# Optimization experiments

Hardware: AMD Instinct MI355X
Metric: run time of the kernel (lower is better)

Reference implementation:

```python
import jax, jax.numpy as jnp
import numpy as np

S = 4  # spixel_downsize


def _shift2d(x, oy, ox):
    # out[..., y, x] = x[..., y - oy, x - ox] if in-bounds else 0 (zero pad)
    pad = [(0, 0)] * (x.ndim - 2) + [(S, S), (S, S)]
    xp = jnp.pad(x, pad)
    h, w = x.shape[-2], x.shape[-1]
    return xp[..., S - oy:S - oy + h, S - ox:S - ox + w]


def _valid_mask(h, w, oy, ox):
    ys = jnp.arange(h)
    xs = jnp.arange(w)
    my = (ys - oy >= 0) & (ys - oy < h)
    mx = (xs - ox >= 0) & (xs - ox < w)
    return my[:, None] & mx[None, :]


def _conv3d(x, w, stride, pad):
    return jax.lax.conv_general_dilated(
        x, w, window_strides=stride, padding=[(p, p) for p in pad],
        dimension_numbers=('NCDHW', 'OIDHW', 'NCDHW'))


def _basic(x, w, stride, pad):
    # BasicConv: Conv3d(bias=False) + BN(identity at init) + ReLU
    return jax.nn.relu(_conv3d(x, w, stride, pad))


def setup_inputs() -> dict:
    key = jax.random.key(0)
    ks = jax.random.split(key, 8)
    cv = jax.random.normal(ks[0], (1, 8, 24, 128, 256), jnp.float32)
    sp = jax.random.uniform(ks[1], (1, 9, 128, 256), jnp.float32)
    xy = jax.random.normal(ks[2], (1, 2, 128, 256), jnp.float32)
    w_stem = jax.random.normal(ks[3], (16, 72, 1, 1, 1), jnp.float32) * 0.05
    w1a = jax.random.normal(ks[4], (32, 16, 3, 2, 2), jnp.float32) * 0.05
    w1b = jax.random.normal(ks[5], (32, 32, 3, 1, 1), jnp.float32) * 0.05
    w2a = jax.random.normal(ks[6], (64, 32, 3, 2, 2), jnp.float32) * 0.05
    w2b = jax.random.normal(ks[7], (64, 64, 3, 1, 1), jnp.float32) * 0.05
    return dict(cv=cv, sp=sp, xy=xy, w_stem=w_stem, w1a=w1a, w1b=w1b, w2a=w2a, w2b=w2b)


def reference(cv, sp, xy, w_stem, w1a, w1b, w2a, w2b):
    b, c, d, h, w = cv.shape
    feats, probs = [], []
    uv0 = jnp.zeros((b, 2, h, w), cv.dtype)
    # 9 shifted neighbors; neighbor k shifts by (S*((k//3)-1), S*((k%3)-1)).
    # All uv writes in the original target slot 0 and sequentially overwrite;
    for k in range(9):
        oy = S * ((k // 3) - 1)
        ox = S * ((k % 3) - 1)
        p = _shift2d(sp[:, k], oy, ox)                      # (b,h,w), zeros outside
        probs.append(p)
        feats.append(_shift2d(cv, oy, ox) * p[:, None, None])  # (b,c,d,h,w)
        u = _shift2d(xy, oy, ox) * p[:, None]               # (b,2,h,w)
        mask = _valid_mask(h, w, oy, ox)[None, None]
        uv0 = jnp.where(mask, u, uv0)
    # (b, c, 9, d, h, w) -> (b, 9c, d, h, w), matching torch reshape order
    feat = jnp.stack(feats, axis=2).reshape(b, c * 9, d, h, w)
    prob_sum = jnp.sum(jnp.stack(probs, axis=1), axis=1, keepdims=True)  # (b,1,h,w)
    tot = prob_sum.reshape(b, 1, h // S, S, w // S, S).mean((3, 5))      # avg_pool2d
    tot_up = jnp.repeat(jnp.repeat(tot, S, axis=2), S, axis=3)           # nearest upsample
    feat = feat / tot_up[:, :, None]                                     # (b,9c,d,h,w)
    feat = _basic(feat, w_stem, (1, 1, 1), (0, 0, 0))
    f1 = _basic(feat, w1a, (2, 2, 2), (1, 0, 0))
    f1 = _basic(f1, w1b, (1, 1, 1), (1, 0, 0))
    f2 = _basic(f1, w2a, (2, 2, 2), (1, 0, 0))
    f2 = _basic(f2, w2b, (1, 1, 1), (1, 0, 0))
    # uv.sum(2) == uv0 since only neighbor-slot 0 is written
    uv = uv0.reshape(b, 2, h // S, S, w // S, S).mean((3, 5)) / tot      # (b,2,h/S,w/S)
    return f1, f2, uv.reshape(b, 2, -1)
```

## Files before the change

### kernel.cpp

```cpp
#include <hip/hip_runtime.h>

#define HH 128
#define WW 256

#define OFF_TOT   0
#define OFF_WT    2048
#define WT_STEM   0
#define WT_1A     1152
#define WT_1B     7296
#define WT_2A     10368
#define WT_2B     34944
#define OFF_STEM  49280
#define OFF_F1A   12632192
#define OFF_F1N   15777920
#define OFF_F2A   49280

__global__ __launch_bounds__(256) void k_pre(
    const float* __restrict__ sp, const float* __restrict__ xy,
    const float* __restrict__ wstem, const float* __restrict__ w1a,
    const float* __restrict__ w1b, const float* __restrict__ w2a,
    const float* __restrict__ w2b,
    float* __restrict__ tot, float* __restrict__ uv_out, float* __restrict__ wt)
{
  int gid = blockIdx.x * 256 + threadIdx.x;
  if (gid < 1152) { int o = gid & 15, r = gid >> 4; int ci = r / 9, k = r - ci * 9;
    wt[WT_STEM + gid] = wstem[o * 72 + ci * 9 + k]; }
  if (gid < 6144) { int o = gid & 31, ci = (gid >> 5) & 15, tp = gid >> 9;
    wt[WT_1A + gid] = w1a[o * 192 + ci * 12 + tp]; }
  if (gid < 3072) { int o = gid & 31, ci = (gid >> 5) & 31, kd = gid >> 10;
    wt[WT_1B + gid] = w1b[(o * 32 + ci) * 3 + kd]; }
  if (gid < 24576) { int o = gid & 63, ci = (gid >> 6) & 31, tp = gid >> 11;
    wt[WT_2A + gid] = w2a[o * 384 + ci * 12 + tp]; }
  if (gid < 12288) { int o = gid & 63, ci = (gid >> 6) & 63, kd = gid >> 12;
    wt[WT_2B + gid] = w2b[(o * 64 + ci) * 3 + kd]; }
  if (gid < 8192) {
    int cell = gid >> 2, q = gid & 3;
    int Y = cell >> 6, X = cell & 63;
    float tsum = 0.f, u0 = 0.f, u1 = 0.f;
    int y = Y * 4 + q;
#pragma unroll
    for (int j = 0; j < 4; ++j) {
      int x = X * 4 + j;
      float psum = 0.f;
#pragma unroll
      for (int k = 0; k < 9; ++k) {
        int oy = 4 * ((k / 3) - 1), ox = 4 * ((k % 3) - 1);
        int sy = y - oy, sx = x - ox;
        if (sy >= 0 && sy < HH && sx >= 0 && sx < WW)
          psum += sp[k * HH * WW + sy * WW + sx];
      }
      tsum += psum;
      int oy = (y >= 4) ? 4 : 0;
      int ox = (x >= 4) ? 4 : 0;
      int kk = (oy ? 2 : 1) * 3 + (ox ? 2 : 1);
      int sy = y - oy, sx = x - ox;
      float p = sp[kk * HH * WW + sy * WW + sx];
      u0 += xy[sy * WW + sx] * p;
      u1 += xy[HH * WW + sy * WW + sx] * p;
    }
    tsum += __shfl_xor(tsum, 1); tsum += __shfl_xor(tsum, 2);
    u0 += __shfl_xor(u0, 1); u0 += __shfl_xor(u0, 2);
    u1 += __shfl_xor(u1, 1); u1 += __shfl_xor(u1, 2);
    if (q == 0) {
      float t = tsum * (1.f / 16.f);
      tot[cell] = t;
      float inv = 1.f / t;
      uv_out[cell] = u0 * (1.f / 16.f) * inv;
      uv_out[2048 + cell] = u1 * (1.f / 16.f) * inv;
    }
  }
}

__global__ __launch_bounds__(256) void k_stem(
    const float* __restrict__ cv, const float* __restrict__ sp,
    const float* __restrict__ wt, const float* __restrict__ tot,
    float* __restrict__ out)
{
  __shared__ float wl[1152];
  for (int i = threadIdx.x; i < 1152; i += 256) wl[i] = wt[i];
  __syncthreads();
  int x0 = blockIdx.x * 128 + 2 * (threadIdx.x & 63);
  int y  = blockIdx.y * 4 + (threadIdx.x >> 6);
  int d  = blockIdx.z;
  float2 p2[9]; int off[9];
#pragma unroll
  for (int k = 0; k < 9; ++k) {
    int oy = 4 * ((k / 3) - 1), ox = 4 * ((k % 3) - 1);
    int sy = y - oy, sx = x0 - ox;
    bool v = (sy >= 0) && (sy < HH) && (sx >= 0) && (sx < WW - 1);
    int syc = v ? sy : 0, sxc = v ? sx : 0;
    off[k] = syc * WW + sxc;
    float2 t = *(const float2*)(sp + k * HH * WW + off[k]);
    p2[k].x = v ? t.x : 0.f;
    p2[k].y = v ? t.y : 0.f;
  }
  float acc[16][2];
#pragma unroll
  for (int o = 0; o < 16; ++o) { acc[o][0] = 0.f; acc[o][1] = 0.f; }
  const float* cvd = cv + (size_t)d * HH * WW;
#pragma unroll
  for (int ci = 0; ci < 8; ++ci) {
    const float* cvp = cvd + (size_t)ci * 24 * HH * WW;
    float2 c2[9];
#pragma unroll
    for (int k = 0; k < 9; ++k) c2[k] = *(const float2*)(cvp + off[k]);
#pragma unroll
    for (int k = 0; k < 9; ++k) {
      float t0 = c2[k].x * p2[k].x, t1 = c2[k].y * p2[k].y;
      const float* wb = &wl[(ci * 9 + k) * 16];
      float wv[16];
#pragma unroll
      for (int q = 0; q < 4; ++q) *(float4*)&wv[q * 4] = *(const float4*)(wb + q * 4);
#pragma unroll
      for (int o = 0; o < 16; ++o) {
        acc[o][0] += wv[o] * t0;
        acc[o][1] += wv[o] * t1;
      }
    }
  }
  float inv = 1.f / tot[(y >> 2) * 64 + (x0 >> 2)];
  float* op = out + (((size_t)d * HH + y) * WW + x0) * 16;
#pragma unroll
  for (int p = 0; p < 2; ++p)
#pragma unroll
    for (int q = 0; q < 4; ++q) {
      float4 v;
      v.x = fmaxf(acc[q * 4 + 0][p] * inv, 0.f);
      v.y = fmaxf(acc[q * 4 + 1][p] * inv, 0.f);
      v.z = fmaxf(acc[q * 4 + 2][p] * inv, 0.f);
      v.w = fmaxf(acc[q * 4 + 3][p] * inv, 0.f);
      *(float4*)(op + p * 16 + q * 4) = v;
    }
}

__global__ __launch_bounds__(256) void k_conv1a(
    const float* __restrict__ in, const float* __restrict__ wt,
    float* __restrict__ out)
{
  __shared__ float wl[6144];
  for (int i = threadIdx.x; i < 6144; i += 256) wl[i] = wt[i];
  __syncthreads();
  int tid = threadIdx.x;
  int xo0 = (blockIdx.x & 1) * 64 + 2 * (tid & 31);
  int yo  = (blockIdx.x >> 1) * 8 + (tid >> 5);
  int dz = blockIdx.y, og = blockIdx.z;
  float acc[16][2];
#pragma unroll
  for (int o = 0; o < 16; ++o) { acc[o][0] = 0.f; acc[o][1] = 0.f; }
  for (int kd = 0; kd < 3; ++kd) {
    int d = 2 * dz - 1 + kd;
    if (d < 0 || d >= 24) continue;
#pragma unroll
    for (int ky = 0; ky < 2; ++ky) {
      int y = 2 * yo + ky;
      float iv[64];
      const float4* ip = (const float4*)(in + (((size_t)d * 128 + y) * 256 + 2 * xo0) * 16);
#pragma unroll
      for (int q = 0; q < 16; ++q) {
        float4 v = ip[q];
        iv[q * 4 + 0] = v.x; iv[q * 4 + 1] = v.y;
        iv[q * 4 + 2] = v.z; iv[q * 4 + 3] = v.w;
      }
#pragma unroll
      for (int kx = 0; kx < 2; ++kx) {
        const float* wtap = &wl[((kd * 2 + ky) * 2 + kx) * 512 + og * 16];
#pragma unroll
        for (int ci = 0; ci < 16; ++ci) {
          const float* wb = wtap + ci * 32;
          float wv[16];
#pragma unroll
          for (int q = 0; q < 4; ++q) *(float4*)&wv[q * 4] = *(const float4*)(wb + q * 4);
          float a0 = iv[(0 + kx) * 16 + ci];
          float a1 = iv[(2 + kx) * 16 + ci];
#pragma unroll
          for (int o = 0; o < 16; ++o) {
            acc[o][0] += wv[o] * a0;
            acc[o][1] += wv[o] * a1;
          }
        }
      }
    }
  }
  float* op = out + (((size_t)dz * 64 + yo) * 128 + xo0) * 32 + og * 16;
#pragma unroll
  for (int p = 0; p < 2; ++p)
#pragma unroll
    for (int q = 0; q < 4; ++q) {
      float4 v;
      v.x = fmaxf(acc[q * 4 + 0][p], 0.f);
      v.y = fmaxf(acc[q * 4 + 1][p], 0.f);
      v.z = fmaxf(acc[q * 4 + 2][p], 0.f);
      v.w = fmaxf(acc[q * 4 + 3][p], 0.f);
      *(float4*)(op + p * 32 + q * 4) = v;
    }
}

__global__ __launch_bounds__(256) void k_conv1b(
    const float* __restrict__ in, const float* __restrict__ wt,
    float* __restrict__ outn, float* __restrict__ outc)
{
  __shared__ float wl[3072];
  for (int i = threadIdx.x; i < 3072; i += 256) wl[i] = wt[i];
  __syncthreads();
  int tid = threadIdx.x;
  int xo = (blockIdx.x & 1) * 64 + (tid & 63);
  int yo = (blockIdx.x >> 1) * 4 + (tid >> 6);
  int dz = blockIdx.y, og = blockIdx.z;
  float acc[16];
#pragma unroll
  for (int o = 0; o < 16; ++o) acc[o] = 0.f;
  for (int kd = 0; kd < 3; ++kd) {
    int d = dz - 1 + kd;
    if (d < 0 || d >= 12) continue;
    float iv[32];
    const float4* ip = (const float4*)(in + (((size_t)d * 64 + yo) * 128 + xo) * 32);
#pragma unroll
    for (int q = 0; q < 8; ++q) {
      float4 v = ip[q];
      iv[q * 4 + 0] = v.x; iv[q * 4 + 1] = v.y;
      iv[q * 4 + 2] = v.z; iv[q * 4 + 3] = v.w;
    }
    const float* wk = &wl[kd * 1024 + og * 16];
#pragma unroll
    for (int ci = 0; ci < 32; ++ci) {
      const float* wb = wk + ci * 32;
      float wv[16];
#pragma unroll
      for (int q = 0; q < 4; ++q) *(float4*)&wv[q * 4] = *(const float4*)(wb + q * 4);
#pragma unroll
      for (int o = 0; o < 16; ++o) acc[o] += wv[o] * iv[ci];
    }
  }
  float* onp = outn + (((size_t)dz * 64 + yo) * 128 + xo) * 32 + og * 16;
#pragma unroll
  for (int q = 0; q < 4; ++q) {
    float4 v;
    v.x = fmaxf(acc[q * 4 + 0], 0.f);
    v.y = fmaxf(acc[q * 4 + 1], 0.f);
    v.z = fmaxf(acc[q * 4 + 2], 0.f);
    v.w = fmaxf(acc[q * 4 + 3], 0.f);
    *(float4*)(onp + q * 4) = v;
  }
#pragma unroll
  for (int o = 0; o < 16; ++o)
    outc[((size_t)((og * 16 + o) * 12 + dz) * 64 + yo) * 128 + xo] = fmaxf(acc[o], 0.f);
}

__global__ __launch_bounds__(256) void k_conv2a(
    const float* __restrict__ in, const float* __restrict__ wt,
    float* __restrict__ out)
{
  __shared__ float wl[3072];
  int og = blockIdx.z;
  for (int i = threadIdx.x; i < 3072; i += 256) {
    int o = i & 7, ci = (i >> 3) & 31, tap = i >> 8;
    wl[i] = wt[tap * 2048 + ci * 64 + og * 8 + o];
  }
  __syncthreads();
  int tid = threadIdx.x;
  int xo = tid & 63;
  int yo = blockIdx.x * 4 + (tid >> 6);
  int dz = blockIdx.y;
  float acc[8];
#pragma unroll
  for (int o = 0; o < 8; ++o) acc[o] = 0.f;
  for (int kd = 0; kd < 3; ++kd) {
    int d = 2 * dz - 1 + kd;
    if (d < 0 || d >= 12) continue;
#pragma unroll
    for (int ky = 0; ky < 2; ++ky) {
      int y = 2 * yo + ky;
      float iv[64];
      const float4* ip = (const float4*)(in + (((size_t)d * 64 + y) * 128 + 2 * xo) * 32);
#pragma unroll
      for (int q = 0; q < 16; ++q) {
        float4 v = ip[q];
        iv[q * 4 + 0] = v.x; iv[q * 4 + 1] = v.y;
        iv[q * 4 + 2] = v.z; iv[q * 4 + 3] = v.w;
      }
#pragma unroll
      for (int kx = 0; kx < 2; ++kx) {
        const float* wtap = &wl[((kd * 2 + ky) * 2 + kx) * 256];
#pragma unroll
        for (int ci = 0; ci < 32; ++ci) {
          const float* wb = wtap + ci * 8;
          float wv[8];
          *(float4*)&wv[0] = *(const float4*)(wb);
          *(float4*)&wv[4] = *(const float4*)(wb + 4);
          float a = iv[kx * 32 + ci];
#pragma unroll
          for (int o = 0; o < 8; ++o) acc[o] += wv[o] * a;
        }
      }
    }
  }
  float* op = out + (((size_t)dz * 32 + yo) * 64 + xo) * 64 + og * 8;
  float4 v0, v1;
  v0.x = fmaxf(acc[0], 0.f); v0.y = fmaxf(acc[1], 0.f);
  v0.z = fmaxf(acc[2], 0.f); v0.w = fmaxf(acc[3], 0.f);
  v1.x = fmaxf(acc[4], 0.f); v1.y = fmaxf(acc[5], 0.f);
  v1.z = fmaxf(acc[6], 0.f); v1.w = fmaxf(acc[7], 0.f);
  *(float4*)op = v0; *(float4*)(op + 4) = v1;
}

__global__ __launch_bounds__(256) void k_conv2b(
    const float* __restrict__ in, const float* __restrict__ wt,
    float* __restrict__ out)
{
  __shared__ float wl[1536];
  int og = blockIdx.z;
  for (int i = threadIdx.x; i < 1536; i += 256) {
    int o = i & 7, ci = (i >> 3) & 63, kd = i >> 9;
    wl[i] = wt[kd * 4096 + ci * 64 + og * 8 + o];
  }
  __syncthreads();
  int tid = threadIdx.x;
  int xo = tid & 63;
  int yo = blockIdx.x * 4 + (tid >> 6);
  int dz = blockIdx.y;
  float acc[8];
#pragma unroll
  for (int o = 0; o < 8; ++o) acc[o] = 0.f;
  for (int kd = 0; kd < 3; ++kd) {
    int d = dz - 1 + kd;
    if (d < 0 || d >= 6) continue;
    float iv[64];
    const float4* ip = (const float4*)(in + (((size_t)d * 32 + yo) * 64 + xo) * 64);
#pragma unroll
    for (int q = 0; q < 16; ++q) {
      float4 v = ip[q];
      iv[q * 4 + 0] = v.x; iv[q * 4 + 1] = v.y;
      iv[q * 4 + 2] = v.z; iv[q * 4 + 3] = v.w;
    }
    const float* wk = &wl[kd * 512];
#pragma unroll
    for (int ci = 0; ci < 64; ++ci) {
      const float* wb = wk + ci * 8;
      float wv[8];
      *(float4*)&wv[0] = *(const float4*)(wb);
      *(float4*)&wv[4] = *(const float4*)(wb + 4);
#pragma unroll
      for (int o = 0; o < 8; ++o) acc[o] += wv[o] * iv[ci];
    }
  }
#pragma unroll
  for (int o = 0; o < 8; ++o)
    out[((size_t)((og * 8 + o) * 6 + dz) * 32 + yo) * 64 + xo] = fmaxf(acc[o], 0.f);
}

extern "C" void kernel_launch(void* const* d_in, const int* in_sizes, int n_in,
                              void* d_out, int out_size, void* d_ws, size_t ws_size,
                              hipStream_t stream) {
  const float* cv    = (const float*)d_in[0];
  const float* sp    = (const float*)d_in[1];
  const float* xy    = (const float*)d_in[2];
  const float* wstem = (const float*)d_in[3];
  const float* w1a   = (const float*)d_in[4];
  const float* w1b   = (const float*)d_in[5];
  const float* w2a   = (const float*)d_in[6];
  const float* w2b   = (const float*)d_in[7];
  float* out = (float*)d_out;
  float* out_f1 = out;
  float* out_f2 = out + 3145728;
  float* out_uv = out + 3145728 + 786432;

  float* ws = (float*)d_ws;
  float* t_tot  = ws + OFF_TOT;
  float* wt     = ws + OFF_WT;
  float* t_stem = ws + OFF_STEM;
  float* t_f1a  = ws + OFF_F1A;
  float* t_f1n  = ws + OFF_F1N;
  float* t_f2a  = ws + OFF_F2A;

  k_pre<<<96, 256, 0, stream>>>(sp, xy, wstem, w1a, w1b, w2a, w2b,
                                t_tot, out_uv, wt);
  k_stem<<<dim3(2, 32, 24), 256, 0, stream>>>(cv, sp, wt + WT_STEM, t_tot, t_stem);
  k_conv1a<<<dim3(16, 12, 2), 256, 0, stream>>>(t_stem, wt + WT_1A, t_f1a);
  k_conv1b<<<dim3(32, 12, 2), 256, 0, stream>>>(t_f1a, wt + WT_1B, t_f1n, out_f1);
  k_conv2a<<<dim3(8, 6, 8), 256, 0, stream>>>(t_f1n, wt + WT_2A, t_f2a);
  k_conv2b<<<dim3(8, 6, 8), 256, 0, stream>>>(t_f2a, wt + WT_2B, out_f2);
}
```

Before: 174.7 us.

## Double-buffer input loads and split output channels across more blocks in conv kernels

Every conv kernel now prefetches the next input slice into registers (a double-buffered `ib[2][32]`) while the current slice is multiplied. The stem kernel does the same across its input channels. Output channels per thread are halved in all four convs (1a: 16→8, 1b: 16→8, 2a/2b: 8→4), and the grids grow to match. This gives more parallelism and lower register pressure, which should raise occupancy and hide load latency, at the cost of rereading each input once per extra channel group.

```diff
diff --git a/kernel.cpp b/kernel.cpp
--- a/kernel.cpp
+++ b/kernel.cpp
@@ -2,6 +2,7 @@
 
 #define HH 128
 #define WW 256
+#define HW (HH * WW)
 
 #define OFF_TOT   0
 #define OFF_WT    2048
@@ -47,16 +48,16 @@
         int oy = 4 * ((k / 3) - 1), ox = 4 * ((k % 3) - 1);
         int sy = y - oy, sx = x - ox;
         if (sy >= 0 && sy < HH && sx >= 0 && sx < WW)
-          psum += sp[k * HH * WW + sy * WW + sx];
+          psum += sp[k * HW + sy * WW + sx];
       }
       tsum += psum;
       int oy = (y >= 4) ? 4 : 0;
       int ox = (x >= 4) ? 4 : 0;
       int kk = (oy ? 2 : 1) * 3 + (ox ? 2 : 1);
       int sy = y - oy, sx = x - ox;
-      float p = sp[kk * HH * WW + sy * WW + sx];
+      float p = sp[kk * HW + sy * WW + sx];
       u0 += xy[sy * WW + sx] * p;
-      u1 += xy[HH * WW + sy * WW + sx] * p;
+      u1 += xy[HW + sy * WW + sx] * p;
     }
     tsum += __shfl_xor(tsum, 1); tsum += __shfl_xor(tsum, 2);
     u0 += __shfl_xor(u0, 1); u0 += __shfl_xor(u0, 2);
@@ -90,23 +91,28 @@
     bool v = (sy >= 0) && (sy < HH) && (sx >= 0) && (sx < WW - 1);
     int syc = v ? sy : 0, sxc = v ? sx : 0;
     off[k] = syc * WW + sxc;
-    float2 t = *(const float2*)(sp + k * HH * WW + off[k]);
+    float2 t = *(const float2*)(sp + k * HW + off[k]);
     p2[k].x = v ? t.x : 0.f;
     p2[k].y = v ? t.y : 0.f;
   }
   float acc[16][2];
 #pragma unroll
   for (int o = 0; o < 16; ++o) { acc[o][0] = 0.f; acc[o][1] = 0.f; }
-  const float* cvd = cv + (size_t)d * HH * WW;
+  const float* cvd = cv + (size_t)d * HW;
+  float2 cb[2][9];
+#pragma unroll
+  for (int k = 0; k < 9; ++k) cb[0][k] = *(const float2*)(cvd + off[k]);
 #pragma unroll
   for (int ci = 0; ci < 8; ++ci) {
-    const float* cvp = cvd + (size_t)ci * 24 * HH * WW;
-    float2 c2[9];
-#pragma unroll
-    for (int k = 0; k < 9; ++k) c2[k] = *(const float2*)(cvp + off[k]);
+    if (ci < 7) {
+#pragma unroll
+      for (int k = 0; k < 9; ++k)
+        cb[(ci + 1) & 1][k] = *(const float2*)(cvd + (size_t)(ci + 1) * 24 * HW + off[k]);
+    }
 #pragma unroll
     for (int k = 0; k < 9; ++k) {
-      float t0 = c2[k].x * p2[k].x, t1 = c2[k].y * p2[k].y;
+      float t0 = cb[ci & 1][k].x * p2[k].x;
+      float t1 = cb[ci & 1][k].y * p2[k].y;
       const float* wb = &wl[(ci * 9 + k) * 16];
       float wv[16];
 #pragma unroll
@@ -137,164 +143,60 @@
     const float* __restrict__ in, const float* __restrict__ wt,
     float* __restrict__ out)
 {
-  __shared__ float wl[6144];
-  for (int i = threadIdx.x; i < 6144; i += 256) wl[i] = wt[i];
+  __shared__ float wl[1536];
+  int og = blockIdx.z;
+  for (int i = threadIdx.x; i < 1536; i += 256) {
+    int o = i & 7, ci = (i >> 3) & 15, tap = i >> 7;
+    wl[i] = wt[tap * 512 + ci * 32 + og * 8 + o];
+  }
   __syncthreads();
-  int tid = threadIdx.x;
-  int xo0 = (blockIdx.x & 1) * 64 + 2 * (tid & 31);
-  int yo  = (blockIdx.x >> 1) * 8 + (tid >> 5);
-  int dz = blockIdx.y, og = blockIdx.z;
-  float acc[16][2];
-#pragma unroll
-  for (int o = 0; o < 16; ++o) { acc[o][0] = 0.f; acc[o][1] = 0.f; }
-  for (int kd = 0; kd < 3; ++kd) {
-    int d = 2 * dz - 1 + kd;
-    if (d < 0 || d >= 24) continue;
-#pragma unroll
-    for (int ky = 0; ky < 2; ++ky) {
-      int y = 2 * yo + ky;
-      float iv[64];
-      const float4* ip = (const float4*)(in + (((size_t)d * 128 + y) * 256 + 2 * xo0) * 16);
-#pragma unroll
-      for (int q = 0; q < 16; ++q) {
-        float4 v = ip[q];
-        iv[q * 4 + 0] = v.x; iv[q * 4 + 1] = v.y;
-        iv[q * 4 + 2] = v.z; iv[q * 4 + 3] = v.w;
-      }
-#pragma unroll
-      for (int kx = 0; kx < 2; ++kx) {
-        const float* wtap = &wl[((kd * 2 + ky) * 2 + kx) * 512 + og * 16];
-#pragma unroll
-        for (int ci = 0; ci < 16; ++ci) {
-          const float* wb = wtap + ci * 32;
-          float wv[16];
-#pragma unroll
-          for (int q = 0; q < 4; ++q) *(float4*)&wv[q * 4] = *(const float4*)(wb + q * 4);
-          float a0 = iv[(0 + kx) * 16 + ci];
-          float a1 = iv[(2 + kx) * 16 + ci];
-#pragma unroll
-          for (int o = 0; o < 16; ++o) {
-            acc[o][0] += wv[o] * a0;
-            acc[o][1] += wv[o] * a1;
-          }
-        }
-      }
-    }
-  }
-  float* op = out + (((size_t)dz * 64 + yo) * 128 + xo0) * 32 + og * 16;
-#pragma unroll
-  for (int p = 0; p < 2; ++p)
-#pragma unroll
-    for (int q = 0; q < 4; ++q) {
-      float4 v;
-      v.x = fmaxf(acc[q * 4 + 0][p], 0.f);
-      v.y = fmaxf(acc[q * 4 + 1][p], 0.f);
-      v.z = fmaxf(acc[q * 4 + 2][p], 0.f);
-      v.w = fmaxf(acc[q * 4 + 3][p], 0.f);
-      *(float4*)(op + p * 32 + q * 4) = v;
-    }
-}
-
-__global__ __launch_bounds__(256) void k_conv1b(
-    const float* __restrict__ in, const float* __restrict__ wt,
-    float* __restrict__ outn, float* __restrict__ outc)
-{
-  __shared__ float wl[3072];
-  for (int i = threadIdx.x; i < 3072; i += 256) wl[i] = wt[i];
-  __syncthreads();
-  int tid = threadIdx.x;
-  int xo = (blockIdx.x & 1) * 64 + (tid & 63);
-  int yo = (blockIdx.x >> 1) * 4 + (tid >> 6);
-  int dz = blockIdx.y, og = blockIdx.z;
-  float acc[16];
-#pragma unroll
-  for (int o = 0; o < 16; ++o) acc[o] = 0.f;
-  for (int kd = 0; kd < 3; ++kd) {
-    int d = dz - 1 + kd;
-    if (d < 0 || d >= 12) continue;
-    float iv[32];
-    const float4* ip = (const float4*)(in + (((size_t)d * 64 + yo) * 128 + xo) * 32);
-#pragma unroll
-    for (int q = 0; q < 8; ++q) {
-      float4 v = ip[q];
-      iv[q * 4 + 0] = v.x; iv[q * 4 + 1] = v.y;
-      iv[q * 4 + 2] = v.z; iv[q * 4 + 3] = v.w;
-    }
-    const float* wk = &wl[kd * 1024 + og * 16];
-#pragma unroll
-    for (int ci = 0; ci < 32; ++ci) {
-      const float* wb = wk + ci * 32;
-      float wv[16];
-#pragma unroll
-      for (int q = 0; q < 4; ++q) *(float4*)&wv[q * 4] = *(const float4*)(wb + q * 4);
-#pragma unroll
-      for (int o = 0; o < 16; ++o) acc[o] += wv[o] * iv[ci];
-    }
-  }
-  float* onp = outn + (((size_t)dz * 64 + yo) * 128 + xo) * 32 + og * 16;
-#pragma unroll
-  for (int q = 0; q < 4; ++q) {
-    float4 v;
-    v.x = fmaxf(acc[q * 4 + 0], 0.f);
-    v.y = fmaxf(acc[q * 4 + 1], 0.f);
-    v.z = fmaxf(acc[q * 4 + 2], 0.f);
-    v.w = fmaxf(acc[q * 4 + 3], 0.f);
-    *(float4*)(onp + q * 4) = v;
-  }
-#pragma unroll
-  for (int o = 0; o < 16; ++o)
-    outc[((size_t)((og * 16 + o) * 12 + dz) * 64 + yo) * 128 + xo] = fmaxf(acc[o], 0.f);
-}
-
-__global__ __launch_bounds__(256) void k_conv2a(
-    const float* __restrict__ in, const float* __restrict__ wt,
-    float* __restrict__ out)
-{
-  __shared__ float wl[3072];
-  int og = blockIdx.z;
-  for (int i = threadIdx.x; i < 3072; i += 256) {
-    int o = i & 7, ci = (i >> 3) & 31, tap = i >> 8;
-    wl[i] = wt[tap * 2048 + ci * 64 + og * 8 + o];
-  }
-  __syncthreads();
-  int tid = threadIdx.x;
-  int xo = tid & 63;
-  int yo = blockIdx.x * 4 + (tid >> 6);
+  int xo = threadIdx.x & 127;
+  int yo = blockIdx.x * 2 + (threadIdx.x >> 7);
   int dz = blockIdx.y;
   float acc[8];
 #pragma unroll
   for (int o = 0; o < 8; ++o) acc[o] = 0.f;
-  for (int kd = 0; kd < 3; ++kd) {
-    int d = 2 * dz - 1 + kd;
-    if (d < 0 || d >= 12) continue;
-#pragma unroll
-    for (int ky = 0; ky < 2; ++ky) {
+  float ib[2][32];
+  {
+    int dd = 2 * dz - 1; dd = dd < 0 ? 0 : dd;
+    const float4* ip = (const float4*)(in + (((size_t)dd * 128 + 2 * yo) * 256 + 2 * xo) * 16);
+#pragma unroll
+    for (int q = 0; q < 8; ++q) {
+      float4 t = ip[q];
+      ib[0][q * 4] = t.x; ib[0][q * 4 + 1] = t.y; ib[0][q * 4 + 2] = t.z; ib[0][q * 4 + 3] = t.w;
+    }
+  }
+#pragma unroll
+  for (int w = 0; w < 6; ++w) {
+    if (w < 5) {
+      int kd = (w + 1) >> 1, ky = (w + 1) & 1;
+      int dd = 2 * dz - 1 + kd; dd = dd < 0 ? 0 : dd;
       int y = 2 * yo + ky;
-      float iv[64];
-      const float4* ip = (const float4*)(in + (((size_t)d * 64 + y) * 128 + 2 * xo) * 32);
-#pragma unroll
-      for (int q = 0; q < 16; ++q) {
-        float4 v = ip[q];
-        iv[q * 4 + 0] = v.x; iv[q * 4 + 1] = v.y;
-        iv[q * 4 + 2] = v.z; iv[q * 4 + 3] = v.w;
-      }
+      const float4* ip = (const float4*)(in + (((size_t)dd * 128 + y) * 256 + 2 * xo) * 16);
+#pragma unroll
+      for (int q = 0; q < 8; ++q) {
+        float4 t = ip[q];
+        ib[(w + 1) & 1][q * 4] = t.x; ib[(w + 1) & 1][q * 4 + 1] = t.y;
+        ib[(w + 1) & 1][q * 4 + 2] = t.z; ib[(w + 1) & 1][q * 4 + 3] = t.w;
+      }
+    }
+    if (2 * dz - 1 + (w >> 1) >= 0) {
 #pragma unroll
       for (int kx = 0; kx < 2; ++kx) {
-        const float* wtap = &wl[((kd * 2 + ky) * 2 + kx) * 256];
-#pragma unroll
-        for (int ci = 0; ci < 32; ++ci) {
-          const float* wb = wtap + ci * 8;
+        const float* wsl = &wl[(w * 2 + kx) * 128];
+#pragma unroll
+        for (int ci = 0; ci < 16; ++ci) {
           float wv[8];
-          *(float4*)&wv[0] = *(const float4*)(wb);
-          *(float4*)&wv[4] = *(const float4*)(wb + 4);
-          float a = iv[kx * 32 + ci];
+          *(float4*)&wv[0] = *(const float4*)(wsl + ci * 8);
+          *(float4*)&wv[4] = *(const float4*)(wsl + ci * 8 + 4);
+          float a = ib[w & 1][kx * 16 + ci];
 #pragma unroll
           for (int o = 0; o < 8; ++o) acc[o] += wv[o] * a;
         }
       }
     }
   }
-  float* op = out + (((size_t)dz * 32 + yo) * 64 + xo) * 64 + og * 8;
+  float* op = out + (((size_t)dz * 64 + yo) * 128 + xo) * 32 + og * 8;
   float4 v0, v1;
   v0.x = fmaxf(acc[0], 0.f); v0.y = fmaxf(acc[1], 0.f);
   v0.z = fmaxf(acc[2], 0.f); v0.w = fmaxf(acc[3], 0.f);
@@ -303,49 +205,184 @@
   *(float4*)op = v0; *(float4*)(op + 4) = v1;
 }
 
+__global__ __launch_bounds__(256) void k_conv1b(
+    const float* __restrict__ in, const float* __restrict__ wt,
+    float* __restrict__ outn, float* __restrict__ outc)
+{
+  __shared__ float wl[768];
+  int og = blockIdx.z;
+  for (int i = threadIdx.x; i < 768; i += 256) {
+    int o = i & 7, ci = (i >> 3) & 31, kd = i >> 8;
+    wl[i] = wt[kd * 1024 + ci * 32 + og * 8 + o];
+  }
+  __syncthreads();
+  int xo = threadIdx.x & 127;
+  int yo = blockIdx.x * 2 + (threadIdx.x >> 7);
+  int dz = blockIdx.y;
+  float acc[8];
+#pragma unroll
+  for (int o = 0; o < 8; ++o) acc[o] = 0.f;
+  float ib[2][32];
+  {
+    int dd = dz - 1; dd = dd < 0 ? 0 : dd;
+    const float4* ip = (const float4*)(in + (((size_t)dd * 64 + yo) * 128 + xo) * 32);
+#pragma unroll
+    for (int q = 0; q < 8; ++q) {
+      float4 t = ip[q];
+      ib[0][q * 4] = t.x; ib[0][q * 4 + 1] = t.y; ib[0][q * 4 + 2] = t.z; ib[0][q * 4 + 3] = t.w;
+    }
+  }
+#pragma unroll
+  for (int w = 0; w < 3; ++w) {
+    if (w < 2) {
+      int dd = dz + w;  dd = dd >= 12 ? 11 : dd;
+      const float4* ip = (const float4*)(in + (((size_t)dd * 64 + yo) * 128 + xo) * 32);
+#pragma unroll
+      for (int q = 0; q < 8; ++q) {
+        float4 t = ip[q];
+        ib[(w + 1) & 1][q * 4] = t.x; ib[(w + 1) & 1][q * 4 + 1] = t.y;
+        ib[(w + 1) & 1][q * 4 + 2] = t.z; ib[(w + 1) & 1][q * 4 + 3] = t.w;
+      }
+    }
+    int d_ = dz - 1 + w;
+    if (d_ >= 0 && d_ < 12) {
+      const float* wsl = &wl[w * 256];
+#pragma unroll
+      for (int ci = 0; ci < 32; ++ci) {
+        float wv[8];
+        *(float4*)&wv[0] = *(const float4*)(wsl + ci * 8);
+        *(float4*)&wv[4] = *(const float4*)(wsl + ci * 8 + 4);
+        float a = ib[w & 1][ci];
+#pragma unroll
+        for (int o = 0; o < 8; ++o) acc[o] += wv[o] * a;
+      }
+    }
+  }
+  float* onp = outn + (((size_t)dz * 64 + yo) * 128 + xo) * 32 + og * 8;
+  float4 v0, v1;
+  v0.x = fmaxf(acc[0], 0.f); v0.y = fmaxf(acc[1], 0.f);
+  v0.z = fmaxf(acc[2], 0.f); v0.w = fmaxf(acc[3], 0.f);
+  v1.x = fmaxf(acc[4], 0.f); v1.y = fmaxf(acc[5], 0.f);
+  v1.z = fmaxf(acc[6], 0.f); v1.w = fmaxf(acc[7], 0.f);
+  *(float4*)onp = v0; *(float4*)(onp + 4) = v1;
+#pragma unroll
+  for (int o = 0; o < 8; ++o)
+    outc[((size_t)((og * 8 + o) * 12 + dz) * 64 + yo) * 128 + xo] = fmaxf(acc[o], 0.f);
+}
+
+__global__ __launch_bounds__(256) void k_conv2a(
+    const float* __restrict__ in, const float* __restrict__ wt,
+    float* __restrict__ out)
+{
+  __shared__ float wl[1536];
+  int og = blockIdx.z;
+  for (int i = threadIdx.x; i < 1536; i += 256) {
+    int o = i & 3, ci = (i >> 2) & 31, tap = i >> 7;
+    wl[i] = wt[tap * 2048 + ci * 64 + og * 4 + o];
+  }
+  __syncthreads();
+  int xo = threadIdx.x & 63;
+  int yo = blockIdx.x * 4 + (threadIdx.x >> 6);
+  int dz = blockIdx.y;
+  float acc[4] = {0.f, 0.f, 0.f, 0.f};
+  float ib[2][32];
+  {
+    int dd = 2 * dz - 1; dd = dd < 0 ? 0 : dd;
+    const float4* ip = (const float4*)(in + (((size_t)dd * 64 + 2 * yo) * 128 + 2 * xo) * 32);
+#pragma unroll
+    for (int q = 0; q < 8; ++q) {
+      float4 t = ip[q];
+      ib[0][q * 4] = t.x; ib[0][q * 4 + 1] = t.y; ib[0][q * 4 + 2] = t.z; ib[0][q * 4 + 3] = t.w;
+    }
+  }
+#pragma unroll
+  for (int w = 0; w < 12; ++w) {
+    if (w < 11) {
+      int wn = w + 1;
+      int kd = wn >> 2, ky = (wn >> 1) & 1, kx = wn & 1;
+      int dd = 2 * dz - 1 + kd; dd = dd < 0 ? 0 : dd;
+      int y = 2 * yo + ky, x = 2 * xo + kx;
+      const float4* ip = (const float4*)(in + (((size_t)dd * 64 + y) * 128 + x) * 32);
+#pragma unroll
+      for (int q = 0; q < 8; ++q) {
+        float4 t = ip[q];
+        ib[wn & 1][q * 4] = t.x; ib[wn & 1][q * 4 + 1] = t.y;
+        ib[wn & 1][q * 4 + 2] = t.z; ib[wn & 1][q * 4 + 3] = t.w;
+      }
+    }
+    if (2 * dz - 1 + (w >> 2) >= 0) {
+      const float* wsl = &wl[w * 128];
+#pragma unroll
+      for (int ci = 0; ci < 32; ++ci) {
+        float wv[4];
+        *(float4*)&wv[0] = *(const float4*)(wsl + ci * 4);
+        float a = ib[w & 1][ci];
+#pragma unroll
+        for (int o = 0; o < 4; ++o) acc[o] += wv[o] * a;
+      }
+    }
+  }
+  float4 v;
+  v.x = fmaxf(acc[0], 0.f); v.y = fmaxf(acc[1], 0.f);
+  v.z = fmaxf(acc[2], 0.f); v.w = fmaxf(acc[3], 0.f);
+  *(float4*)(out + (((size_t)dz * 32 + yo) * 64 + xo) * 64 + og * 4) = v;
+}
+
 __global__ __launch_bounds__(256) void k_conv2b(
     const float* __restrict__ in, const float* __restrict__ wt,
     float* __restrict__ out)
 {
-  __shared__ float wl[1536];
+  __shared__ float wl[768];
   int og = blockIdx.z;
-  for (int i = threadIdx.x; i < 1536; i += 256) {
-    int o = i & 7, ci = (i >> 3) & 63, kd = i >> 9;
-    wl[i] = wt[kd * 4096 + ci * 64 + og * 8 + o];
+  for (int i = threadIdx.x; i < 768; i += 256) {
+    int o = i & 3, ci = (i >> 2) & 63, kd = i >> 8;
+    wl[i] = wt[kd * 4096 + ci * 64 + og * 4 + o];
   }
   __syncthreads();
-  int tid = threadIdx.x;
-  int xo = tid & 63;
-  int yo = blockIdx.x * 4 + (tid >> 6);
+  int xo = threadIdx.x & 63;
+  int yo = blockIdx.x * 4 + (threadIdx.x >> 6);
   int dz = blockIdx.y;
-  float acc[8];
-#pragma unroll
-  for (int o = 0; o < 8; ++o) acc[o] = 0.f;
-  for (int kd = 0; kd < 3; ++kd) {
-    int d = dz - 1 + kd;
-    if (d < 0 || d >= 6) continue;
-    float iv[64];
-    const float4* ip = (const float4*)(in + (((size_t)d * 32 + yo) * 64 + xo) * 64);
-#pragma unroll
-    for (int q = 0; q < 16; ++q) {
-      float4 v = ip[q];
-      iv[q * 4 + 0] = v.x; iv[q * 4 + 1] = v.y;
-      iv[q * 4 + 2] = v.z; iv[q * 4 + 3] = v.w;
-    }
-    const float* wk = &wl[kd * 512];
-#pragma unroll
-    for (int ci = 0; ci < 64; ++ci) {
-      const float* wb = wk + ci * 8;
-      float wv[8];
-      *(float4*)&wv[0] = *(const float4*)(wb);
-      *(float4*)&wv[4] = *(const float4*)(wb + 4);
-#pragma unroll
-      for (int o = 0; o < 8; ++o) acc[o] += wv[o] * iv[ci];
-    }
-  }
-#pragma unroll
-  for (int o = 0; o < 8; ++o)
-    out[((size_t)((og * 8 + o) * 6 + dz) * 32 + yo) * 64 + xo] = fmaxf(acc[o], 0.f);
+  float acc[4] = {0.f, 0.f, 0.f, 0.f};
+  float ib[2][32];
+  {
+    int dd = dz - 1; dd = dd < 0 ? 0 : dd;
+    const float4* ip = (const float4*)(in + (((size_t)dd * 32 + yo) * 64 + xo) * 64);
+#pragma unroll
+    for (int q = 0; q < 8; ++q) {
+      float4 t = ip[q];
+      ib[0][q * 4] = t.x; ib[0][q * 4 + 1] = t.y; ib[0][q * 4 + 2] = t.z; ib[0][q * 4 + 3] = t.w;
+    }
+  }
+#pragma unroll
+  for (int w = 0; w < 6; ++w) {
+    if (w < 5) {
+      int wn = w + 1;
+      int kd = wn >> 1, hf = wn & 1;
+      int dd = dz - 1 + kd; dd = dd < 0 ? 0 : (dd >= 6 ? 5 : dd);
+      const float4* ip = (const float4*)(in + (((size_t)dd * 32 + yo) * 64 + xo) * 64 + hf * 32);
+#pragma unroll
+      for (int q = 0; q < 8; ++q) {
+        float4 t = ip[q];
+        ib[wn & 1][q * 4] = t.x; ib[wn & 1][q * 4 + 1] = t.y;
+        ib[wn & 1][q * 4 + 2] = t.z; ib[wn & 1][q * 4 + 3] = t.w;
+      }
+    }
+    int d_ = dz - 1 + (w >> 1);
+    if (d_ >= 0 && d_ < 6) {
+      const float* wsl = &wl[w * 128];
+#pragma unroll
+      for (int ci = 0; ci < 32; ++ci) {
+        float wv[4];
+        *(float4*)&wv[0] = *(const float4*)(wsl + ci * 4);
+        float a = ib[w & 1][ci];
+#pragma unroll
+        for (int o = 0; o < 4; ++o) acc[o] += wv[o] * a;
+      }
+    }
+  }
+#pragma unroll
+  for (int o = 0; o < 4; ++o)
+    out[((size_t)((og * 4 + o) * 6 + dz) * 32 + yo) * 64 + xo] = fmaxf(acc[o], 0.f);
 }
 
 extern "C" void kernel_launch(void* const* d_in, const int* in_sizes, int n_in,
@@ -375,8 +412,8 @@
   k_pre<<<96, 256, 0, stream>>>(sp, xy, wstem, w1a, w1b, w2a, w2b,
                                 t_tot, out_uv, wt);
   k_stem<<<dim3(2, 32, 24), 256, 0, stream>>>(cv, sp, wt + WT_STEM, t_tot, t_stem);
-  k_conv1a<<<dim3(16, 12, 2), 256, 0, stream>>>(t_stem, wt + WT_1A, t_f1a);
-  k_conv1b<<<dim3(32, 12, 2), 256, 0, stream>>>(t_f1a, wt + WT_1B, t_f1n, out_f1);
-  k_conv2a<<<dim3(8, 6, 8), 256, 0, stream>>>(t_f1n, wt + WT_2A, t_f2a);
-  k_conv2b<<<dim3(8, 6, 8), 256, 0, stream>>>(t_f2a, wt + WT_2B, out_f2);
-}
+  k_conv1a<<<dim3(32, 12, 4), 256, 0, stream>>>(t_stem, wt + WT_1A, t_f1a);
+  k_conv1b<<<dim3(32, 12, 4), 256, 0, stream>>>(t_f1a, wt + WT_1B, t_f1n, out_f1);
+  k_conv2a<<<dim3(8, 6, 16), 256, 0, stream>>>(t_f1n, wt + WT_2A, t_f2a);
+  k_conv2b<<<dim3(8, 6, 16), 256, 0, stream>>>(t_f2a, wt + WT_2B, out_f2);
+}
```

Result: slower. 181.6 us (+4.0%).

## Retile stem and conv1 kernels into 8-output-channel groups with depth-pair and double buffering

Applied to the files above, without the earlier changes.

The stem kernel now computes 8 output channels per block across two depth planes, sharing the shifted probability weights between them. It also double-buffers the cost-volume loads across input channels. Conv1a and conv1b are split into 8-channel output groups with two pixels per thread, which shrinks shared-memory weight tiles and accumulator registers and raises occupancy. The trade-off is more input re-reads per output group (more blocks each read the same activations) in exchange for lower register pressure and more parallelism.

```diff
diff --git a/kernel.cpp b/kernel.cpp
--- a/kernel.cpp
+++ b/kernel.cpp
@@ -2,6 +2,7 @@
 
 #define HH 128
 #define WW 256
+#define HW (HH * WW)
 
 #define OFF_TOT   0
 #define OFF_WT    2048
@@ -47,16 +48,16 @@
         int oy = 4 * ((k / 3) - 1), ox = 4 * ((k % 3) - 1);
         int sy = y - oy, sx = x - ox;
         if (sy >= 0 && sy < HH && sx >= 0 && sx < WW)
-          psum += sp[k * HH * WW + sy * WW + sx];
+          psum += sp[k * HW + sy * WW + sx];
       }
       tsum += psum;
       int oy = (y >= 4) ? 4 : 0;
       int ox = (x >= 4) ? 4 : 0;
       int kk = (oy ? 2 : 1) * 3 + (ox ? 2 : 1);
       int sy = y - oy, sx = x - ox;
-      float p = sp[kk * HH * WW + sy * WW + sx];
+      float p = sp[kk * HW + sy * WW + sx];
       u0 += xy[sy * WW + sx] * p;
-      u1 += xy[HH * WW + sy * WW + sx] * p;
+      u1 += xy[HW + sy * WW + sx] * p;
     }
     tsum += __shfl_xor(tsum, 1); tsum += __shfl_xor(tsum, 2);
     u0 += __shfl_xor(u0, 1); u0 += __shfl_xor(u0, 2);
@@ -76,104 +77,128 @@
     const float* __restrict__ wt, const float* __restrict__ tot,
     float* __restrict__ out)
 {
-  __shared__ float wl[1152];
-  for (int i = threadIdx.x; i < 1152; i += 256) wl[i] = wt[i];
+  __shared__ float wl[576];
+  int og = blockIdx.x & 1;
+  int xh = blockIdx.x >> 1;
+  for (int i = threadIdx.x; i < 576; i += 256)
+    wl[i] = wt[(i >> 3) * 16 + og * 8 + (i & 7)];
   __syncthreads();
-  int x0 = blockIdx.x * 128 + 2 * (threadIdx.x & 63);
+  int x0 = xh * 128 + 2 * (threadIdx.x & 63);
   int y  = blockIdx.y * 4 + (threadIdx.x >> 6);
-  int d  = blockIdx.z;
+  int d0 = blockIdx.z * 2;
   float2 p2[9]; int off[9];
 #pragma unroll
   for (int k = 0; k < 9; ++k) {
     int oy = 4 * ((k / 3) - 1), ox = 4 * ((k % 3) - 1);
     int sy = y - oy, sx = x0 - ox;
-    bool v = (sy >= 0) && (sy < HH) && (sx >= 0) && (sx < WW - 1);
+    bool v = (sy >= 0) && (sy < HH) && (sx >= 0) && (sx <= WW - 2);
     int syc = v ? sy : 0, sxc = v ? sx : 0;
     off[k] = syc * WW + sxc;
-    float2 t = *(const float2*)(sp + k * HH * WW + off[k]);
+    float2 t = *(const float2*)(sp + k * HW + off[k]);
     p2[k].x = v ? t.x : 0.f;
     p2[k].y = v ? t.y : 0.f;
   }
-  float acc[16][2];
-#pragma unroll
-  for (int o = 0; o < 16; ++o) { acc[o][0] = 0.f; acc[o][1] = 0.f; }
-  const float* cvd = cv + (size_t)d * HH * WW;
+  float acc[8][2][2];
+#pragma unroll
+  for (int o = 0; o < 8; ++o)
+#pragma unroll
+    for (int pl = 0; pl < 2; ++pl) { acc[o][pl][0] = 0.f; acc[o][pl][1] = 0.f; }
+  const float* cvd = cv + (size_t)d0 * HW;
+  float2 cb[2][2][9];
+#pragma unroll
+  for (int pl = 0; pl < 2; ++pl)
+#pragma unroll
+    for (int k = 0; k < 9; ++k)
+      cb[0][pl][k] = *(const float2*)(cvd + (size_t)pl * HW + off[k]);
 #pragma unroll
   for (int ci = 0; ci < 8; ++ci) {
-    const float* cvp = cvd + (size_t)ci * 24 * HH * WW;
-    float2 c2[9];
-#pragma unroll
-    for (int k = 0; k < 9; ++k) c2[k] = *(const float2*)(cvp + off[k]);
+    if (ci < 7) {
+#pragma unroll
+      for (int pl = 0; pl < 2; ++pl)
+#pragma unroll
+        for (int k = 0; k < 9; ++k)
+          cb[(ci + 1) & 1][pl][k] =
+            *(const float2*)(cvd + (size_t)(ci + 1) * 24 * HW + (size_t)pl * HW + off[k]);
+    }
 #pragma unroll
     for (int k = 0; k < 9; ++k) {
-      float t0 = c2[k].x * p2[k].x, t1 = c2[k].y * p2[k].y;
-      const float* wb = &wl[(ci * 9 + k) * 16];
-      float wv[16];
-#pragma unroll
-      for (int q = 0; q < 4; ++q) *(float4*)&wv[q * 4] = *(const float4*)(wb + q * 4);
-#pragma unroll
-      for (int o = 0; o < 16; ++o) {
-        acc[o][0] += wv[o] * t0;
-        acc[o][1] += wv[o] * t1;
+      float t00 = cb[ci & 1][0][k].x * p2[k].x;
+      float t01 = cb[ci & 1][0][k].y * p2[k].y;
+      float t10 = cb[ci & 1][1][k].x * p2[k].x;
+      float t11 = cb[ci & 1][1][k].y * p2[k].y;
+      const float* wb = &wl[(ci * 9 + k) * 8];
+      float wv[8];
+      *(float4*)&wv[0] = *(const float4*)wb;
+      *(float4*)&wv[4] = *(const float4*)(wb + 4);
+#pragma unroll
+      for (int o = 0; o < 8; ++o) {
+        acc[o][0][0] += wv[o] * t00;
+        acc[o][0][1] += wv[o] * t01;
+        acc[o][1][0] += wv[o] * t10;
+        acc[o][1][1] += wv[o] * t11;
       }
     }
   }
   float inv = 1.f / tot[(y >> 2) * 64 + (x0 >> 2)];
-  float* op = out + (((size_t)d * HH + y) * WW + x0) * 16;
-#pragma unroll
-  for (int p = 0; p < 2; ++p)
-#pragma unroll
-    for (int q = 0; q < 4; ++q) {
-      float4 v;
-      v.x = fmaxf(acc[q * 4 + 0][p] * inv, 0.f);
-      v.y = fmaxf(acc[q * 4 + 1][p] * inv, 0.f);
-      v.z = fmaxf(acc[q * 4 + 2][p] * inv, 0.f);
-      v.w = fmaxf(acc[q * 4 + 3][p] * inv, 0.f);
-      *(float4*)(op + p * 16 + q * 4) = v;
-    }
+#pragma unroll
+  for (int pl = 0; pl < 2; ++pl) {
+    float* op = out + (((size_t)(d0 + pl) * HH + y) * WW + x0) * 16 + og * 8;
+#pragma unroll
+    for (int px = 0; px < 2; ++px) {
+      float4 v0, v1;
+      v0.x = fmaxf(acc[0][pl][px] * inv, 0.f); v0.y = fmaxf(acc[1][pl][px] * inv, 0.f);
+      v0.z = fmaxf(acc[2][pl][px] * inv, 0.f); v0.w = fmaxf(acc[3][pl][px] * inv, 0.f);
+      v1.x = fmaxf(acc[4][pl][px] * inv, 0.f); v1.y = fmaxf(acc[5][pl][px] * inv, 0.f);
+      v1.z = fmaxf(acc[6][pl][px] * inv, 0.f); v1.w = fmaxf(acc[7][pl][px] * inv, 0.f);
+      *(float4*)(op + px * 16) = v0;
+      *(float4*)(op + px * 16 + 4) = v1;
+    }
+  }
 }
 
 __global__ __launch_bounds__(256) void k_conv1a(
     const float* __restrict__ in, const float* __restrict__ wt,
     float* __restrict__ out)
 {
-  __shared__ float wl[6144];
-  for (int i = threadIdx.x; i < 6144; i += 256) wl[i] = wt[i];
+  __shared__ float wl[1536];
+  int og = blockIdx.z;
+  for (int i = threadIdx.x; i < 1536; i += 256) {
+    int o = i & 7, ci = (i >> 3) & 15, tap = i >> 7;
+    wl[i] = wt[tap * 512 + ci * 32 + og * 8 + o];
+  }
   __syncthreads();
-  int tid = threadIdx.x;
-  int xo0 = (blockIdx.x & 1) * 64 + 2 * (tid & 31);
-  int yo  = (blockIdx.x >> 1) * 8 + (tid >> 5);
-  int dz = blockIdx.y, og = blockIdx.z;
-  float acc[16][2];
-#pragma unroll
-  for (int o = 0; o < 16; ++o) { acc[o][0] = 0.f; acc[o][1] = 0.f; }
+  int xq = threadIdx.x & 63;
+  int yo = blockIdx.x * 4 + (threadIdx.x >> 6);
+  int dz = blockIdx.y;
+  float acc[8][2];
+#pragma unroll
+  for (int o = 0; o < 8; ++o) { acc[o][0] = 0.f; acc[o][1] = 0.f; }
   for (int kd = 0; kd < 3; ++kd) {
     int d = 2 * dz - 1 + kd;
     if (d < 0 || d >= 24) continue;
 #pragma unroll
     for (int ky = 0; ky < 2; ++ky) {
       int y = 2 * yo + ky;
-      float iv[64];
-      const float4* ip = (const float4*)(in + (((size_t)d * 128 + y) * 256 + 2 * xo0) * 16);
+      float ib[64];
+      const float4* ip = (const float4*)(in + (((size_t)d * 128 + y) * 256 + 4 * xq) * 16);
 #pragma unroll
       for (int q = 0; q < 16; ++q) {
-        float4 v = ip[q];
-        iv[q * 4 + 0] = v.x; iv[q * 4 + 1] = v.y;
-        iv[q * 4 + 2] = v.z; iv[q * 4 + 3] = v.w;
+        float4 t = ip[q];
+        ib[q * 4] = t.x; ib[q * 4 + 1] = t.y; ib[q * 4 + 2] = t.z; ib[q * 4 + 3] = t.w;
       }
 #pragma unroll
       for (int kx = 0; kx < 2; ++kx) {
-        const float* wtap = &wl[((kd * 2 + ky) * 2 + kx) * 512 + og * 16];
+        const float* wtap = &wl[((kd * 2 + ky) * 2 + kx) * 128];
 #pragma unroll
         for (int ci = 0; ci < 16; ++ci) {
-          const float* wb = wtap + ci * 32;
-          float wv[16];
-#pragma unroll
-          for (int q = 0; q < 4; ++q) *(float4*)&wv[q * 4] = *(const float4*)(wb + q * 4);
-          float a0 = iv[(0 + kx) * 16 + ci];
-          float a1 = iv[(2 + kx) * 16 + ci];
-#pragma unroll
-          for (int o = 0; o < 16; ++o) {
+          const float* wb = wtap + ci * 8;
+          float wv[8];
+          *(float4*)&wv[0] = *(const float4*)wb;
+          *(float4*)&wv[4] = *(const float4*)(wb + 4);
+          float a0 = ib[(0 + kx) * 16 + ci];
+          float a1 = ib[(2 + kx) * 16 + ci];
+#pragma unroll
+          for (int o = 0; o < 8; ++o) {
             acc[o][0] += wv[o] * a0;
             acc[o][1] += wv[o] * a1;
           }
@@ -181,69 +206,80 @@
       }
     }
   }
-  float* op = out + (((size_t)dz * 64 + yo) * 128 + xo0) * 32 + og * 16;
-#pragma unroll
-  for (int p = 0; p < 2; ++p)
-#pragma unroll
-    for (int q = 0; q < 4; ++q) {
-      float4 v;
-      v.x = fmaxf(acc[q * 4 + 0][p], 0.f);
-      v.y = fmaxf(acc[q * 4 + 1][p], 0.f);
-      v.z = fmaxf(acc[q * 4 + 2][p], 0.f);
-      v.w = fmaxf(acc[q * 4 + 3][p], 0.f);
-      *(float4*)(op + p * 32 + q * 4) = v;
-    }
+  float* op = out + (((size_t)dz * 64 + yo) * 128 + 2 * xq) * 32 + og * 8;
+#pragma unroll
+  for (int px = 0; px < 2; ++px) {
+    float4 v0, v1;
+    v0.x = fmaxf(acc[0][px], 0.f); v0.y = fmaxf(acc[1][px], 0.f);
+    v0.z = fmaxf(acc[2][px], 0.f); v0.w = fmaxf(acc[3][px], 0.f);
+    v1.x = fmaxf(acc[4][px], 0.f); v1.y = fmaxf(acc[5][px], 0.f);
+    v1.z = fmaxf(acc[6][px], 0.f); v1.w = fmaxf(acc[7][px], 0.f);
+    *(float4*)(op + px * 32) = v0;
+    *(float4*)(op + px * 32 + 4) = v1;
+  }
 }
 
 __global__ __launch_bounds__(256) void k_conv1b(
     const float* __restrict__ in, const float* __restrict__ wt,
     float* __restrict__ outn, float* __restrict__ outc)
 {
-  __shared__ float wl[3072];
-  for (int i = threadIdx.x; i < 3072; i += 256) wl[i] = wt[i];
+  __shared__ float wl[768];
+  int og = blockIdx.z;
+  for (int i = threadIdx.x; i < 768; i += 256) {
+    int o = i & 7, ci = (i >> 3) & 31, kd = i >> 8;
+    wl[i] = wt[kd * 1024 + ci * 32 + og * 8 + o];
+  }
   __syncthreads();
-  int tid = threadIdx.x;
-  int xo = (blockIdx.x & 1) * 64 + (tid & 63);
-  int yo = (blockIdx.x >> 1) * 4 + (tid >> 6);
-  int dz = blockIdx.y, og = blockIdx.z;
-  float acc[16];
-#pragma unroll
-  for (int o = 0; o < 16; ++o) acc[o] = 0.f;
+  int xq = threadIdx.x & 63;
+  int yo = blockIdx.x * 4 + (threadIdx.x >> 6);
+  int dz = blockIdx.y;
+  float acc[8][2];
+#pragma unroll
+  for (int o = 0; o < 8; ++o) { acc[o][0] = 0.f; acc[o][1] = 0.f; }
   for (int kd = 0; kd < 3; ++kd) {
     int d = dz - 1 + kd;
     if (d < 0 || d >= 12) continue;
-    float iv[32];
-    const float4* ip = (const float4*)(in + (((size_t)d * 64 + yo) * 128 + xo) * 32);
-#pragma unroll
-    for (int q = 0; q < 8; ++q) {
-      float4 v = ip[q];
-      iv[q * 4 + 0] = v.x; iv[q * 4 + 1] = v.y;
-      iv[q * 4 + 2] = v.z; iv[q * 4 + 3] = v.w;
-    }
-    const float* wk = &wl[kd * 1024 + og * 16];
+    float ib[64];
+    const float4* ip = (const float4*)(in + (((size_t)d * 64 + yo) * 128 + 2 * xq) * 32);
+#pragma unroll
+    for (int q = 0; q < 16; ++q) {
+      float4 t = ip[q];
+      ib[q * 4] = t.x; ib[q * 4 + 1] = t.y; ib[q * 4 + 2] = t.z; ib[q * 4 + 3] = t.w;
+    }
+    const float* wk = &wl[kd * 256];
 #pragma unroll
     for (int ci = 0; ci < 32; ++ci) {
-      const float* wb = wk + ci * 32;
-      float wv[16];
-#pragma unroll
-      for (int q = 0; q < 4; ++q) *(float4*)&wv[q * 4] = *(const float4*)(wb + q * 4);
-#pragma unroll
-      for (int o = 0; o < 16; ++o) acc[o] += wv[o] * iv[ci];
-    }
-  }
-  float* onp = outn + (((size_t)dz * 64 + yo) * 128 + xo) * 32 + og * 16;
-#pragma unroll
-  for (int q = 0; q < 4; ++q) {
-    float4 v;
-    v.x = fmaxf(acc[q * 4 + 0], 0.f);
-    v.y = fmaxf(acc[q * 4 + 1], 0.f);
-    v.z = fmaxf(acc[q * 4 + 2], 0.f);
-    v.w = fmaxf(acc[q * 4 + 3], 0.f);
-    *(float4*)(onp + q * 4) = v;
-  }
-#pragma unroll
-  for (int o = 0; o < 16; ++o)
-    outc[((size_t)((og * 16 + o) * 12 + dz) * 64 + yo) * 128 + xo] = fmaxf(acc[o], 0.f);
+      const float* wb = wk + ci * 8;
+      float wv[8];
+      *(float4*)&wv[0] = *(const float4*)wb;
+      *(float4*)&wv[4] = *(const float4*)(wb + 4);
+      float a0 = ib[ci];
+      float a1 = ib[32 + ci];
+#pragma unroll
+      for (int o = 0; o < 8; ++o) {
+        acc[o][0] += wv[o] * a0;
+        acc[o][1] += wv[o] * a1;
+      }
+    }
+  }
+  float* onp = outn + (((size_t)dz * 64 + yo) * 128 + 2 * xq) * 32 + og * 8;
+#pragma unroll
+  for (int px = 0; px < 2; ++px) {
+    float4 v0, v1;
+    v0.x = fmaxf(acc[0][px], 0.f); v0.y = fmaxf(acc[1][px], 0.f);
+    v0.z = fmaxf(acc[2][px], 0.f); v0.w = fmaxf(acc[3][px], 0.f);
+    v1.x = fmaxf(acc[4][px], 0.f); v1.y = fmaxf(acc[5][px], 0.f);
+    v1.z = fmaxf(acc[6][px], 0.f); v1.w = fmaxf(acc[7][px], 0.f);
+    *(float4*)(onp + px * 32) = v0;
+    *(float4*)(onp + px * 32 + 4) = v1;
+  }
+#pragma unroll
+  for (int o = 0; o < 8; ++o) {
+    float2 v;
+    v.x = fmaxf(acc[o][0], 0.f);
+    v.y = fmaxf(acc[o][1], 0.f);
+    *(float2*)(outc + (((size_t)(og * 8 + o) * 12 + dz) * 64 + yo) * 128 + 2 * xq) = v;
+  }
 }
 
 __global__ __launch_bounds__(256) void k_conv2a(
@@ -257,9 +293,8 @@
     wl[i] = wt[tap * 2048 + ci * 64 + og * 8 + o];
   }
   __syncthreads();
-  int tid = threadIdx.x;
-  int xo = tid & 63;
-  int yo = blockIdx.x * 4 + (tid >> 6);
+  int xo = threadIdx.x & 63;
+  int yo = blockIdx.x * 4 + (threadIdx.x >> 6);
   int dz = blockIdx.y;
   float acc[8];
 #pragma unroll
@@ -270,13 +305,12 @@
 #pragma unroll
     for (int ky = 0; ky < 2; ++ky) {
       int y = 2 * yo + ky;
-      float iv[64];
+      float ib[64];
       const float4* ip = (const float4*)(in + (((size_t)d * 64 + y) * 128 + 2 * xo) * 32);
 #pragma unroll
       for (int q = 0; q < 16; ++q) {
-        float4 v = ip[q];
-        iv[q * 4 + 0] = v.x; iv[q * 4 + 1] = v.y;
-        iv[q * 4 + 2] = v.z; iv[q * 4 + 3] = v.w;
+        float4 t = ip[q];
+        ib[q * 4] = t.x; ib[q * 4 + 1] = t.y; ib[q * 4 + 2] = t.z; ib[q * 4 + 3] = t.w;
       }
 #pragma unroll
       for (int kx = 0; kx < 2; ++kx) {
@@ -285,9 +319,9 @@
         for (int ci = 0; ci < 32; ++ci) {
           const float* wb = wtap + ci * 8;
           float wv[8];
-          *(float4*)&wv[0] = *(const float4*)(wb);
+          *(float4*)&wv[0] = *(const float4*)wb;
           *(float4*)&wv[4] = *(const float4*)(wb + 4);
-          float a = iv[kx * 32 + ci];
+          float a = ib[kx * 32 + ci];
 #pragma unroll
           for (int o = 0; o < 8; ++o) acc[o] += wv[o] * a;
         }
@@ -314,9 +348,8 @@
     wl[i] = wt[kd * 4096 + ci * 64 + og * 8 + o];
   }
   __syncthreads();
-  int tid = threadIdx.x;
-  int xo = tid & 63;
-  int yo = blockIdx.x * 4 + (tid >> 6);
+  int xo = threadIdx.x & 63;
+  int yo = blockIdx.x * 4 + (threadIdx.x >> 6);
   int dz = blockIdx.y;
   float acc[8];
 #pragma unroll
@@ -324,23 +357,23 @@
   for (int kd = 0; kd < 3; ++kd) {
     int d = dz - 1 + kd;
     if (d < 0 || d >= 6) continue;
-    float iv[64];
+    float ib[64];
     const float4* ip = (const float4*)(in + (((size_t)d * 32 + yo) * 64 + xo) * 64);
 #pragma unroll
     for (int q = 0; q < 16; ++q) {
-      float4 v = ip[q];
-      iv[q * 4 + 0] = v.x; iv[q * 4 + 1] = v.y;
-      iv[q * 4 + 2] = v.z; iv[q * 4 + 3] = v.w;
+      float4 t = ip[q];
+      ib[q * 4] = t.x; ib[q * 4 + 1] = t.y; ib[q * 4 + 2] = t.z; ib[q * 4 + 3] = t.w;
     }
     const float* wk = &wl[kd * 512];
 #pragma unroll
     for (int ci = 0; ci < 64; ++ci) {
       const float* wb = wk + ci * 8;
       float wv[8];
-      *(float4*)&wv[0] = *(const float4*)(wb);
+      *(float4*)&wv[0] = *(const float4*)wb;
       *(float4*)&wv[4] = *(const float4*)(wb + 4);
-#pragma unroll
-      for (int o = 0; o < 8; ++o) acc[o] += wv[o] * iv[ci];
+      float a = ib[ci];
+#pragma unroll
+      for (int o = 0; o < 8; ++o) acc[o] += wv[o] * a;
     }
   }
 #pragma unroll
@@ -374,9 +407,9 @@
 
   k_pre<<<96, 256, 0, stream>>>(sp, xy, wstem, w1a, w1b, w2a, w2b,
                                 t_tot, out_uv, wt);
-  k_stem<<<dim3(2, 32, 24), 256, 0, stream>>>(cv, sp, wt + WT_STEM, t_tot, t_stem);
-  k_conv1a<<<dim3(16, 12, 2), 256, 0, stream>>>(t_stem, wt + WT_1A, t_f1a);
-  k_conv1b<<<dim3(32, 12, 2), 256, 0, stream>>>(t_f1a, wt + WT_1B, t_f1n, out_f1);
+  k_stem<<<dim3(4, 32, 12), 256, 0, stream>>>(cv, sp, wt + WT_STEM, t_tot, t_stem);
+  k_conv1a<<<dim3(16, 12, 4), 256, 0, stream>>>(t_stem, wt + WT_1A, t_f1a);
+  k_conv1b<<<dim3(16, 12, 4), 256, 0, stream>>>(t_f1a, wt + WT_1B, t_f1n, out_f1);
   k_conv2a<<<dim3(8, 6, 8), 256, 0, stream>>>(t_f1n, wt + WT_2A, t_f2a);
   k_conv2b<<<dim3(8, 6, 8), 256, 0, stream>>>(t_f2a, wt + WT_2B, out_f2);
 }
```

New measurement: 237.7 us. +36.0%, slower.
